# Kernel tuning notes

Hardware: AMD Instinct MI355X
Metric: run time of the kernel (lower is better)

## Reference

```python
import jax, jax.numpy as jnp
import numpy as np

N, C_IN, T, V = 16, 64, 512, 22
C_OUT = 256
INTER = C_OUT // 4  # coff_embedding = 4


def setup_inputs() -> dict:
    key = jax.random.key(0)
    ks = jax.random.split(key, 8)
    x = jax.random.normal(ks[0], (N, C_IN, T, V), dtype=jnp.float32)
    A = jax.random.uniform(ks[1], (N, T, V, V), dtype=jnp.float32)
    # 1x1 conv weights (only subset 0 is used in forward)
    Wa = jax.random.normal(ks[2], (INTER, C_IN), dtype=jnp.float32) * (2.0 / C_IN) ** 0.5
    ba = jnp.zeros((INTER,), dtype=jnp.float32)
    Wb = jax.random.normal(ks[3], (INTER, C_IN), dtype=jnp.float32) * (2.0 / C_IN) ** 0.5
    bb = jnp.zeros((INTER,), dtype=jnp.float32)
    Wd = jax.random.normal(ks[4], (C_OUT, C_IN), dtype=jnp.float32) * (2.0 / (C_OUT * 3)) ** 0.5
    bd = jnp.zeros((C_OUT,), dtype=jnp.float32)
    return {"x": x, "A": A, "Wa": Wa, "ba": ba, "Wb": Wb, "bb": bb, "Wd": Wd, "bd": bd}


def reference(x, A, Wa, ba, Wb, bb, Wd, bd):
    # x: (N,C,T,V); A: (N,T,V,V). All T frames batched (original loops over t).
    inter = Wa.shape[0]
    # 1x1 convs over channel dim
    A1 = jnp.einsum('ic,nctv->nitv', Wa, x) + ba[None, :, None, None]  # (N,inter,T,V)
    A2 = jnp.einsum('ic,nctv->nitv', Wb, x) + bb[None, :, None, None]
    # scores[n,t,u,v] = sum_i A1[n,i,t,u] * A2[n,i,t,v], scaled by inter channels
    scores = jnp.einsum('nitu,nitv->ntuv', A1, A2) / inter
    # torch Softmax(dim=-2): over rows (u axis)
    A_dyn = jax.nn.softmax(scores, axis=-2)
    # forward-created PA is constant 1e-6 added to A
    A_comb = A + 1e-6 + A_dyn  # (N,T,V,V)
    # graph aggregation: z[n,c,t,u] = sum_w A_comb[n,t,u,w] * x[n,c,t,w]
    z = jnp.einsum('ntuw,nctw->nctu', A_comb, x)
    out = jnp.einsum('oc,nctv->notv', Wd, z) + bd[None, :, None, None]  # (N,C_out,T,V)
    return jax.nn.relu(out)
```

## Files before the change

kernel.cpp:

```cpp
#include <hip/hip_runtime.h>

#define NB    16
#define CIN   64
#define TT    512
#define VV    22
#define COUT  256
#define TBK   4
#define NTB   (TT / TBK)
#define ZROW  (TBK * VV)
#define PAD   24
#define OPAD  23

typedef __attribute__((ext_vector_type(8))) short bf16x8;
typedef __attribute__((ext_vector_type(4))) float f32x4;

__device__ __forceinline__ ushort f2bf(float f) {
    unsigned u = __float_as_uint(f);
    return (ushort)((u + 0x7FFFu + ((u >> 16) & 1u)) >> 16);
}
__device__ __forceinline__ uint pk2(float a, float b) {
    return (uint)f2bf(a) | ((uint)f2bf(b) << 16);
}

__global__ void w_to_bf16(const float* __restrict__ Wa, const float* __restrict__ Wb,
                          const float* __restrict__ Wd,
                          ushort* __restrict__ WaB, ushort* __restrict__ WbB,
                          ushort* __restrict__ WdB)
{
    int i = blockIdx.x * 256 + threadIdx.x;
    if (i < CIN * CIN)                 WaB[i] = f2bf(Wa[i]);
    else if (i < 2 * CIN * CIN)        WbB[i - CIN * CIN] = f2bf(Wb[i - CIN * CIN]);
    else if (i < 2 * CIN * CIN + COUT * CIN)
                                       WdB[i - 2 * CIN * CIN] = f2bf(Wd[i - 2 * CIN * CIN]);
}

__global__ __launch_bounds__(256, 3) void agcn_fused_mfma(
    const float* __restrict__ x, const float* __restrict__ A,
    const ushort* __restrict__ WaB, const float* __restrict__ ba,
    const ushort* __restrict__ WbB, const float* __restrict__ bb,
    const ushort* __restrict__ WdB, const float* __restrict__ bd,
    float* __restrict__ out)
{
    const int bx = blockIdx.x;
    const int tq = (bx & 7) * 16 + (bx >> 3);
    const int n  = blockIdx.y;
    const int tid = threadIdx.x;
    const int lane = tid & 63, wave = tid >> 6;
    const int hi = lane >> 4, lo = lane & 15;
    const int t0 = tq * TBK;

    __shared__ __align__(16) ushort xsb[TBK * 64 * 32];
    __shared__ __align__(16) ushort frag[11264];
    ushort* xbf   = frag;
    ushort* A1bf  = frag;
    ushort* A2bf  = frag + 5632;
    ushort* z_lds = frag;
    ushort* psb   = frag + 6144;
    ushort* zbf   = xsb;

    for (int i = tid; i < TBK * 64 * 5; i += 256) {
        int row = i / 5, q = i - row * 5;
        reinterpret_cast<uint*>(&xsb[row * 32 + 22])[q] = 0u;
    }

    {
        const float* xsrc = x + ((size_t)n * CIN * TT + t0) * VV;
        for (int i4 = tid; i4 < CIN * 22; i4 += 256) {
            int c = i4 / 22, q = i4 - c * 22;
            float4 v4 = *reinterpret_cast<const float4*>(xsrc + (size_t)c * (TT * VV) + q * 4);
            #pragma unroll
            for (int j = 0; j < 4; ++j) {
                int e  = q * 4 + j;
                int tt = e / 22, v = e - tt * 22;
                float val = (j == 0) ? v4.x : (j == 1) ? v4.y : (j == 2) ? v4.z : v4.w;
                xsb[(tt * 64 + c) * 32 + v] = f2bf(val);
            }
        }
    }
    __syncthreads();

    for (int it = tid; it < 1024; it += 256) {
        int kb = it >> 9;
        int t  = (it >> 7) & 3;
        int nt = (it >> 6) & 1;
        int ln = it & 63;
        int v  = nt * 16 + (ln & 15);
        int c0 = kb * 32 + (ln >> 4) * 8;
        ushort tmp[8];
        #pragma unroll
        for (int j = 0; j < 8; ++j) tmp[j] = xsb[(t * 64 + c0 + j) * 32 + v];
        *reinterpret_cast<uint4*>(&xbf[(size_t)it * 8]) = *reinterpret_cast<const uint4*>(tmp);
    }
    __syncthreads();

    f32x4 acc_a[TBK][2], acc_b[TBK][2];
    {
        const int m0 = wave * 16;
        float bav[4], bbv[4];
        #pragma unroll
        for (int r = 0; r < 4; ++r) { bav[r] = ba[m0 + hi * 4 + r]; bbv[r] = bb[m0 + hi * 4 + r]; }
        #pragma unroll
        for (int t = 0; t < TBK; ++t)
            #pragma unroll
            for (int nt = 0; nt < 2; ++nt)
                #pragma unroll
                for (int r = 0; r < 4; ++r) { acc_a[t][nt][r] = bav[r]; acc_b[t][nt][r] = bbv[r]; }
        #pragma unroll
        for (int kb = 0; kb < 2; ++kb) {
            bf16x8 awa = *reinterpret_cast<const bf16x8*>(&WaB[(size_t)(m0 + lo) * CIN + kb * 32 + hi * 8]);
            bf16x8 awb = *reinterpret_cast<const bf16x8*>(&WbB[(size_t)(m0 + lo) * CIN + kb * 32 + hi * 8]);
            #pragma unroll
            for (int t = 0; t < TBK; ++t) {
                #pragma unroll
                for (int nt = 0; nt < 2; ++nt) {
                    bf16x8 bf = *reinterpret_cast<const bf16x8*>(
                        &xbf[(((size_t)(kb * 4 + t) * 2 + nt) * 64 + lane) * 8]);
                    acc_a[t][nt] = __builtin_amdgcn_mfma_f32_16x16x32_bf16(awa, bf, acc_a[t][nt], 0, 0, 0);
                    acc_b[t][nt] = __builtin_amdgcn_mfma_f32_16x16x32_bf16(awb, bf, acc_b[t][nt], 0, 0, 0);
                }
            }
        }
    }
    __syncthreads();

    {
        const int m0 = wave * 16;
        #pragma unroll
        for (int t = 0; t < TBK; ++t) {
            #pragma unroll
            for (int nt = 0; nt < 2; ++nt) {
                const int u = nt * 16 + lo;
                if (u < VV) {
                    uint2 va = {pk2(acc_a[t][nt][0], acc_a[t][nt][1]),
                                pk2(acc_a[t][nt][2], acc_a[t][nt][3])};
                    uint2 vb = {pk2(acc_b[t][nt][0], acc_b[t][nt][1]),
                                pk2(acc_b[t][nt][2], acc_b[t][nt][3])};
                    *reinterpret_cast<uint2*>(&A1bf[((size_t)t * VV + u) * 64 + m0 + hi * 4]) = va;
                    *reinterpret_cast<uint2*>(&A2bf[((size_t)t * VV + u) * 64 + m0 + hi * 4]) = vb;
                }
            }
        }
    }
    __syncthreads();

    f32x4 s[2][2];
    {
        const int t = wave;
        bf16x8 zfrag;
        #pragma unroll
        for (int j = 0; j < 8; ++j) zfrag[j] = 0;
        #pragma unroll
        for (int mt = 0; mt < 2; ++mt)
            #pragma unroll
            for (int nt = 0; nt < 2; ++nt)
                #pragma unroll
                for (int r = 0; r < 4; ++r) s[mt][nt][r] = 0.f;
        #pragma unroll
        for (int kb = 0; kb < 2; ++kb) {
            bf16x8 a[2], b2[2];
            #pragma unroll
            for (int mt = 0; mt < 2; ++mt) {
                const int row = mt * 16 + lo;
                a[mt] = (row < VV) ? *reinterpret_cast<const bf16x8*>(
                            &A1bf[((size_t)t * VV + row) * 64 + kb * 32 + hi * 8]) : zfrag;
            }
            #pragma unroll
            for (int nt = 0; nt < 2; ++nt) {
                const int row = nt * 16 + lo;
                b2[nt] = (row < VV) ? *reinterpret_cast<const bf16x8*>(
                            &A2bf[((size_t)t * VV + row) * 64 + kb * 32 + hi * 8]) : zfrag;
            }
            #pragma unroll
            for (int mt = 0; mt < 2; ++mt)
                #pragma unroll
                for (int nt = 0; nt < 2; ++nt)
                    s[mt][nt] = __builtin_amdgcn_mfma_f32_16x16x32_bf16(a[mt], b2[nt], s[mt][nt], 0, 0, 0);
        }
    }
    __syncthreads();

    {
        const int t = wave;
        bf16x8 zfrag;
        #pragma unroll
        for (int j = 0; j < 8; ++j) zfrag[j] = 0;

        {
            uint* pz = reinterpret_cast<uint*>(psb + (size_t)t * VV * 32);
            #pragma unroll
            for (int i = 0; i < 6; ++i) {
                int idx = i * 64 + lane;
                if (idx < (VV * 32) / 2) pz[idx] = 0u;
            }
        }

        float m[2] = {-1e30f, -1e30f};
        #pragma unroll
        for (int mt = 0; mt < 2; ++mt)
            #pragma unroll
            for (int nt = 0; nt < 2; ++nt)
                #pragma unroll
                for (int r = 0; r < 4; ++r) {
                    s[mt][nt][r] *= (1.0f / 64.0f);
                    const int u = mt * 16 + hi * 4 + r;
                    if (u < VV) m[nt] = fmaxf(m[nt], s[mt][nt][r]);
                }
        #pragma unroll
        for (int nt = 0; nt < 2; ++nt) {
            m[nt] = fmaxf(m[nt], __shfl_xor(m[nt], 16));
            m[nt] = fmaxf(m[nt], __shfl_xor(m[nt], 32));
        }
        float e[2][2][4];
        float sum[2] = {0.f, 0.f};
        #pragma unroll
        for (int mt = 0; mt < 2; ++mt)
            #pragma unroll
            for (int nt = 0; nt < 2; ++nt)
                #pragma unroll
                for (int r = 0; r < 4; ++r) {
                    const int u = mt * 16 + hi * 4 + r;
                    float ev = (u < VV) ? __expf(s[mt][nt][r] - m[nt]) : 0.f;
                    e[mt][nt][r] = ev;
                    sum[nt] += ev;
                }
        #pragma unroll
        for (int nt = 0; nt < 2; ++nt) {
            sum[nt] += __shfl_xor(sum[nt], 16);
            sum[nt] += __shfl_xor(sum[nt], 32);
        }

        {
            const float* Ag = A + ((size_t)(n * TT + t0 + t) * VV) * VV;
            #pragma unroll
            for (int nt = 0; nt < 2; ++nt) {
                const int v = nt * 16 + lo;
                if (v < VV) {
                    const float inv = 1.0f / sum[nt];
                    #pragma unroll
                    for (int mt = 0; mt < 2; ++mt)
                        #pragma unroll
                        for (int r = 0; r < 4; ++r) {
                            const int u = mt * 16 + hi * 4 + r;
                            if (u < VV)
                                psb[((size_t)t * VV + u) * 32 + v] =
                                    f2bf(Ag[u * VV + v] + 1e-6f + e[mt][nt][r] * inv);
                        }
                }
            }
        }
        {
            bf16x8 bfr[2];
            #pragma unroll
            for (int nt = 0; nt < 2; ++nt) {
                const int u = nt * 16 + lo;
                bfr[nt] = (u < VV) ? *reinterpret_cast<const bf16x8*>(
                              &psb[((size_t)t * VV + u) * 32 + hi * 8]) : zfrag;
            }
            #pragma unroll
            for (int mt = 0; mt < 4; ++mt) {
                bf16x8 a = *reinterpret_cast<const bf16x8*>(
                    &xsb[((size_t)(t * 64 + mt * 16 + lo)) * 32 + hi * 8]);
                #pragma unroll
                for (int nt = 0; nt < 2; ++nt) {
                    f32x4 acc = {0.f, 0.f, 0.f, 0.f};
                    acc = __builtin_amdgcn_mfma_f32_16x16x32_bf16(a, bfr[nt], acc, 0, 0, 0);
                    const int u = nt * 16 + lo;
                    if (u < VV) {
                        #pragma unroll
                        for (int r = 0; r < 4; ++r) {
                            const int c = mt * 16 + hi * 4 + r;
                            z_lds[(size_t)c * 96 + t * VV + u] = f2bf(acc[r]);
                        }
                    }
                }
            }
        }
    }
    __syncthreads();

    for (int it = tid; it < 768; it += 256) {
        const int kb  = it / 384;
        const int rem = it - kb * 384;
        const int nt  = rem >> 6;
        const int ln  = rem & 63;
        const int tv  = nt * 16 + (ln & 15);
        const int c0  = kb * 32 + (ln >> 4) * 8;
        ushort tmp[8];
        if (tv < ZROW) {
            #pragma unroll
            for (int j = 0; j < 8; ++j) tmp[j] = z_lds[(size_t)(c0 + j) * 96 + tv];
        } else {
            #pragma unroll
            for (int j = 0; j < 8; ++j) tmp[j] = 0;
        }
        *reinterpret_cast<uint4*>(&zbf[(size_t)it * 8]) = *reinterpret_cast<const uint4*>(tmp);
    }
    __syncthreads();

    {
        const int o0 = wave * 64;
        f32x4 acc[4][6];
        #pragma unroll
        for (int mt = 0; mt < 4; ++mt) {
            #pragma unroll
            for (int r = 0; r < 4; ++r) {
                const float b = bd[o0 + mt * 16 + hi * 4 + r];
                #pragma unroll
                for (int nt = 0; nt < 6; ++nt) acc[mt][nt][r] = b;
            }
        }
        #pragma unroll
        for (int kb = 0; kb < 2; ++kb) {
            bf16x8 bfr[6];
            #pragma unroll
            for (int nt = 0; nt < 6; ++nt)
                bfr[nt] = *reinterpret_cast<const bf16x8*>(&zbf[((kb * 6 + nt) * 64 + lane) * 8]);
            #pragma unroll
            for (int mt = 0; mt < 4; ++mt) {
                bf16x8 aw = *reinterpret_cast<const bf16x8*>(
                    &WdB[(size_t)(o0 + mt * 16 + lo) * CIN + kb * 32 + hi * 8]);
                #pragma unroll
                for (int nt = 0; nt < 6; ++nt)
                    acc[mt][nt] = __builtin_amdgcn_mfma_f32_16x16x32_bf16(aw, bfr[nt], acc[mt][nt], 0, 0, 0);
            }
        }
        #pragma unroll
        for (int mt = 0; mt < 4; ++mt) {
            #pragma unroll
            for (int nt = 0; nt < 6; ++nt) {
                const int col = nt * 16 + lo;
                if (col < ZROW) {
                    #pragma unroll
                    for (int r = 0; r < 4; ++r) {
                        const int o = o0 + mt * 16 + hi * 4 + r;
                        out[((size_t)(n * COUT + o)) * (TT * VV) + (size_t)tq * ZROW + col]
                            = fmaxf(acc[mt][nt][r], 0.f);
                    }
                }
            }
        }
    }
}

__global__ __launch_bounds__(256, 4) void agcn_fused(
    const float* __restrict__ x, const float* __restrict__ A,
    const float* __restrict__ Wa, const float* __restrict__ ba,
    const float* __restrict__ Wb, const float* __restrict__ bb,
    const float* __restrict__ Wd, const float* __restrict__ bd,
    float* __restrict__ out)
{
    const int t   = blockIdx.x;
    const int n   = blockIdx.y;
    const int tid = threadIdx.x;
    __shared__ float smem[7424];
    float* xs   = smem;
    float* A1s  = smem + 1536;
    float* A2s  = smem + 3072;
    float* Ssf  = smem + 4608;
    float* Psf  = smem + 5136;
    float* outs = smem;
    float* zs   = smem + 5888;

    for (int f = tid; f < CIN * VV; f += 256) {
        int c = f / VV, v = f - c * VV;
        xs[c * PAD + v] = x[(((size_t)n * CIN + c) * TT + t) * VV + v];
    }
    {
        const float* Ag = A + (((size_t)n * TT + t) * VV) * VV;
        for (int f = tid; f < VV * VV; f += 256) {
            int u = f / VV, v = f - u * VV;
            Psf[u * PAD + v] = Ag[f] + 1e-6f;
        }
    }
    __syncthreads();
    {
        const int r  = tid & 63;
        const int q  = tid >> 6;
        const int us = (q * VV) >> 2;
        const int ue = ((q + 1) * VV) >> 2;
        const float* War = Wa + r * CIN;
        const float* Wbr = Wb + r * CIN;
        float acc1[6], acc2[6];
        const float b1 = ba[r], b2 = bb[r];
        #pragma unroll
        for (int u = 0; u < 6; ++u) { acc1[u] = b1; acc2[u] = b2; }
        for (int c = 0; c < CIN; c += 4) {
            float4 wa4 = *reinterpret_cast<const float4*>(War + c);
            float4 wb4 = *reinterpret_cast<const float4*>(Wbr + c);
            #pragma unroll
            for (int u = 0; u < 6; ++u) {
                float x0 = xs[(c + 0) * PAD + us + u];
                float x1 = xs[(c + 1) * PAD + us + u];
                float x2 = xs[(c + 2) * PAD + us + u];
                float x3 = xs[(c + 3) * PAD + us + u];
                acc1[u] += wa4.x * x0 + wa4.y * x1 + wa4.z * x2 + wa4.w * x3;
                acc2[u] += wb4.x * x0 + wb4.y * x1 + wb4.z * x2 + wb4.w * x3;
            }
        }
        #pragma unroll
        for (int u = 0; u < 6; ++u) {
            if (us + u < ue) {
                A1s[r * PAD + us + u] = acc1[u];
                A2s[r * PAD + us + u] = acc2[u];
            }
        }
    }
    __syncthreads();
    for (int f = tid; f < VV * VV; f += 256) {
        int u = f / VV, v = f - u * VV;
        float s = 0.f;
        for (int i = 0; i < CIN; ++i)
            s += A1s[i * PAD + u] * A2s[i * PAD + v];
        Ssf[u * PAD + v] = s * (1.0f / 64.0f);
    }
    __syncthreads();
    if (tid < VV) {
        const int v = tid;
        float m = -1e30f;
        #pragma unroll
        for (int u = 0; u < VV; ++u) m = fmaxf(m, Ssf[u * PAD + v]);
        float sum = 0.f;
        #pragma unroll
        for (int u = 0; u < VV; ++u) sum += __expf(Ssf[u * PAD + v] - m);
        const float inv = 1.0f / sum;
        #pragma unroll
        for (int u = 0; u < VV; ++u)
            Psf[u * PAD + v] += __expf(Ssf[u * PAD + v] - m) * inv;
    }
    __syncthreads();
    for (int f = tid; f < CIN * VV; f += 256) {
        int c = f / VV, u = f - c * VV;
        float s = 0.f;
        #pragma unroll
        for (int w = 0; w < VV; ++w)
            s += Psf[u * PAD + w] * xs[c * PAD + w];
        zs[c * PAD + u] = s;
    }
    __syncthreads();
    {
        const int o = tid;
        const float* Wr = Wd + o * CIN;
        float acc[VV];
        const float b = bd[o];
        #pragma unroll
        for (int u = 0; u < VV; ++u) acc[u] = b;
        for (int c = 0; c < CIN; c += 4) {
            float4 w4 = *reinterpret_cast<const float4*>(Wr + c);
            #pragma unroll
            for (int cc = 0; cc < 4; ++cc) {
                const float w = (cc == 0) ? w4.x : (cc == 1) ? w4.y : (cc == 2) ? w4.z : w4.w;
                const float* zr = zs + (c + cc) * PAD;
                #pragma unroll
                for (int uq = 0; uq < 5; ++uq) {
                    float4 zq = *reinterpret_cast<const float4*>(zr + uq * 4);
                    acc[uq * 4 + 0] += w * zq.x;
                    acc[uq * 4 + 1] += w * zq.y;
                    acc[uq * 4 + 2] += w * zq.z;
                    acc[uq * 4 + 3] += w * zq.w;
                }
                float2 zt = *reinterpret_cast<const float2*>(zr + 20);
                acc[20] += w * zt.x;
                acc[21] += w * zt.y;
            }
        }
        #pragma unroll
        for (int u = 0; u < VV; ++u)
            outs[o * OPAD + u] = fmaxf(acc[u], 0.f);
    }
    __syncthreads();
    {
        const size_t obase = (size_t)n * COUT * TT * VV + (size_t)t * VV;
        for (int f = tid; f < COUT * VV; f += 256) {
            int o = f / VV, u = f - o * VV;
            out[obase + (size_t)o * (TT * VV) + u] = outs[o * OPAD + u];
        }
    }
}

extern "C" void kernel_launch(void* const* d_in, const int* in_sizes, int n_in,
                              void* d_out, int out_size, void* d_ws, size_t ws_size,
                              hipStream_t stream) {
    const float* x  = (const float*)d_in[0];
    const float* A  = (const float*)d_in[1];
    const float* Wa = (const float*)d_in[2];
    const float* ba = (const float*)d_in[3];
    const float* Wb = (const float*)d_in[4];
    const float* bb = (const float*)d_in[5];
    const float* Wd = (const float*)d_in[6];
    const float* bd = (const float*)d_in[7];
    float* outp     = (float*)d_out;

    const size_t wab_bytes = (size_t)CIN * CIN * sizeof(ushort);
    const size_t wdb_bytes = (size_t)COUT * CIN * sizeof(ushort);

    if (ws_size >= 2 * wab_bytes + wdb_bytes) {
        ushort* wab = (ushort*)d_ws;
        ushort* wbb = (ushort*)((char*)d_ws + wab_bytes);
        ushort* wdb = (ushort*)((char*)d_ws + 2 * wab_bytes);
        const int prep_items = 2 * CIN * CIN + COUT * CIN;
        w_to_bf16<<<(prep_items + 255) / 256, 256, 0, stream>>>(Wa, Wb, Wd, wab, wbb, wdb);
        dim3 g(NTB, NB);
        agcn_fused_mfma<<<g, 256, 0, stream>>>(x, A, wab, ba, wbb, bb, wdb, bd, outp);
    } else {
        dim3 grid(TT, NB);
        agcn_fused<<<grid, 256, 0, stream>>>(x, A, Wa, ba, Wb, bb, Wd, bd, outp);
    }
}
```

Before: 75.03 us.

## Process eight frames per block with 512 threads and split A1/A2 projections across waves

Doubles the temporal tile from 4 to 8 frames per block and doubles the block to 512 threads (8 waves). Half the waves compute the Wa projection and half the Wb projection instead of each wave computing both. With 176 columns fitting exactly into 11 MFMA tiles, the final Wd GEMM drops its padded columns and loops over column tiles, which reduces register pressure and makes output rows longer and contiguous. The cost is twice the LDS per block and fewer blocks (1024), which may lower occupancy and latency hiding.

```diff
diff --git a/kernel.cpp b/kernel.cpp
--- a/kernel.cpp
+++ b/kernel.cpp
@@ -5,7 +5,7 @@
 #define TT    512
 #define VV    22
 #define COUT  256
-#define TBK   4
+#define TBK   8
 #define NTB   (TT / TBK)
 #define ZROW  (TBK * VV)
 #define PAD   24
@@ -34,7 +34,7 @@
                                        WdB[i - 2 * CIN * CIN] = f2bf(Wd[i - 2 * CIN * CIN]);
 }
 
-__global__ __launch_bounds__(256, 3) void agcn_fused_mfma(
+__global__ __launch_bounds__(512, 2) void agcn_fused_mfma(
     const float* __restrict__ x, const float* __restrict__ A,
     const ushort* __restrict__ WaB, const float* __restrict__ ba,
     const ushort* __restrict__ WbB, const float* __restrict__ bb,
@@ -42,7 +42,7 @@
     float* __restrict__ out)
 {
     const int bx = blockIdx.x;
-    const int tq = (bx & 7) * 16 + (bx >> 3);
+    const int tq = (bx & 7) * 8 + (bx >> 3);
     const int n  = blockIdx.y;
     const int tid = threadIdx.x;
     const int lane = tid & 63, wave = tid >> 6;
@@ -50,23 +50,23 @@
     const int t0 = tq * TBK;
 
     __shared__ __align__(16) ushort xsb[TBK * 64 * 32];
-    __shared__ __align__(16) ushort frag[11264];
+    __shared__ __align__(16) ushort frag[22528];
     ushort* xbf   = frag;
     ushort* A1bf  = frag;
-    ushort* A2bf  = frag + 5632;
+    ushort* A2bf  = frag + 11264;
     ushort* z_lds = frag;
-    ushort* psb   = frag + 6144;
+    ushort* psb   = frag + 11264;
     ushort* zbf   = xsb;
 
-    for (int i = tid; i < TBK * 64 * 5; i += 256) {
+    for (int i = tid; i < TBK * 64 * 5; i += 512) {
         int row = i / 5, q = i - row * 5;
         reinterpret_cast<uint*>(&xsb[row * 32 + 22])[q] = 0u;
     }
 
     {
         const float* xsrc = x + ((size_t)n * CIN * TT + t0) * VV;
-        for (int i4 = tid; i4 < CIN * 22; i4 += 256) {
-            int c = i4 / 22, q = i4 - c * 22;
+        for (int i4 = tid; i4 < CIN * 44; i4 += 512) {
+            int c = i4 / 44, q = i4 - c * 44;
             float4 v4 = *reinterpret_cast<const float4*>(xsrc + (size_t)c * (TT * VV) + q * 4);
             #pragma unroll
             for (int j = 0; j < 4; ++j) {
@@ -79,9 +79,9 @@
     }
     __syncthreads();
 
-    for (int it = tid; it < 1024; it += 256) {
-        int kb = it >> 9;
-        int t  = (it >> 7) & 3;
+    for (int it = tid; it < 2048; it += 512) {
+        int kb = it >> 10;
+        int t  = (it >> 7) & 7;
         int nt = (it >> 6) & 1;
         int ln = it & 63;
         int v  = nt * 16 + (ln & 15);
@@ -93,50 +93,50 @@
     }
     __syncthreads();
 
-    f32x4 acc_a[TBK][2], acc_b[TBK][2];
-    {
-        const int m0 = wave * 16;
-        float bav[4], bbv[4];
-        #pragma unroll
-        for (int r = 0; r < 4; ++r) { bav[r] = ba[m0 + hi * 4 + r]; bbv[r] = bb[m0 + hi * 4 + r]; }
+    f32x4 acc[TBK][2];
+    {
+        const int isB = wave >> 2;
+        const int m0  = (wave & 3) * 16;
+        const ushort* W  = isB ? WbB : WaB;
+        const float*  bv = isB ? bb  : ba;
+        float bias[4];
+        #pragma unroll
+        for (int r = 0; r < 4; ++r) bias[r] = bv[m0 + hi * 4 + r];
         #pragma unroll
         for (int t = 0; t < TBK; ++t)
             #pragma unroll
             for (int nt = 0; nt < 2; ++nt)
                 #pragma unroll
-                for (int r = 0; r < 4; ++r) { acc_a[t][nt][r] = bav[r]; acc_b[t][nt][r] = bbv[r]; }
+                for (int r = 0; r < 4; ++r) acc[t][nt][r] = bias[r];
         #pragma unroll
         for (int kb = 0; kb < 2; ++kb) {
-            bf16x8 awa = *reinterpret_cast<const bf16x8*>(&WaB[(size_t)(m0 + lo) * CIN + kb * 32 + hi * 8]);
-            bf16x8 awb = *reinterpret_cast<const bf16x8*>(&WbB[(size_t)(m0 + lo) * CIN + kb * 32 + hi * 8]);
+            bf16x8 aw = *reinterpret_cast<const bf16x8*>(&W[(size_t)(m0 + lo) * CIN + kb * 32 + hi * 8]);
             #pragma unroll
             for (int t = 0; t < TBK; ++t) {
                 #pragma unroll
                 for (int nt = 0; nt < 2; ++nt) {
                     bf16x8 bf = *reinterpret_cast<const bf16x8*>(
-                        &xbf[(((size_t)(kb * 4 + t) * 2 + nt) * 64 + lane) * 8]);
-                    acc_a[t][nt] = __builtin_amdgcn_mfma_f32_16x16x32_bf16(awa, bf, acc_a[t][nt], 0, 0, 0);
-                    acc_b[t][nt] = __builtin_amdgcn_mfma_f32_16x16x32_bf16(awb, bf, acc_b[t][nt], 0, 0, 0);
-                }
-            }
-        }
-    }
-    __syncthreads();
-
-    {
-        const int m0 = wave * 16;
+                        &xbf[(((size_t)(kb * 8 + t) * 2 + nt) * 64 + lane) * 8]);
+                    acc[t][nt] = __builtin_amdgcn_mfma_f32_16x16x32_bf16(aw, bf, acc[t][nt], 0, 0, 0);
+                }
+            }
+        }
+    }
+    __syncthreads();
+
+    {
+        const int isB = wave >> 2;
+        const int m0  = (wave & 3) * 16;
+        ushort* dst = isB ? A2bf : A1bf;
         #pragma unroll
         for (int t = 0; t < TBK; ++t) {
             #pragma unroll
             for (int nt = 0; nt < 2; ++nt) {
                 const int u = nt * 16 + lo;
                 if (u < VV) {
-                    uint2 va = {pk2(acc_a[t][nt][0], acc_a[t][nt][1]),
-                                pk2(acc_a[t][nt][2], acc_a[t][nt][3])};
-                    uint2 vb = {pk2(acc_b[t][nt][0], acc_b[t][nt][1]),
-                                pk2(acc_b[t][nt][2], acc_b[t][nt][3])};
-                    *reinterpret_cast<uint2*>(&A1bf[((size_t)t * VV + u) * 64 + m0 + hi * 4]) = va;
-                    *reinterpret_cast<uint2*>(&A2bf[((size_t)t * VV + u) * 64 + m0 + hi * 4]) = vb;
+                    uint2 va = {pk2(acc[t][nt][0], acc[t][nt][1]),
+                                pk2(acc[t][nt][2], acc[t][nt][3])};
+                    *reinterpret_cast<uint2*>(&dst[((size_t)t * VV + u) * 64 + m0 + hi * 4]) = va;
                 }
             }
         }
@@ -262,14 +262,14 @@
                     &xsb[((size_t)(t * 64 + mt * 16 + lo)) * 32 + hi * 8]);
                 #pragma unroll
                 for (int nt = 0; nt < 2; ++nt) {
-                    f32x4 acc = {0.f, 0.f, 0.f, 0.f};
-                    acc = __builtin_amdgcn_mfma_f32_16x16x32_bf16(a, bfr[nt], acc, 0, 0, 0);
+                    f32x4 acc4 = {0.f, 0.f, 0.f, 0.f};
+                    acc4 = __builtin_amdgcn_mfma_f32_16x16x32_bf16(a, bfr[nt], acc4, 0, 0, 0);
                     const int u = nt * 16 + lo;
                     if (u < VV) {
                         #pragma unroll
                         for (int r = 0; r < 4; ++r) {
                             const int c = mt * 16 + hi * 4 + r;
-                            z_lds[(size_t)c * 96 + t * VV + u] = f2bf(acc[r]);
+                            z_lds[(size_t)c * ZROW + t * VV + u] = f2bf(acc4[r]);
                         }
                     }
                 }
@@ -278,64 +278,57 @@
     }
     __syncthreads();
 
-    for (int it = tid; it < 768; it += 256) {
-        const int kb  = it / 384;
-        const int rem = it - kb * 384;
+    for (int it = tid; it < 1408; it += 512) {
+        const int kb  = it / 704;
+        const int rem = it - kb * 704;
         const int nt  = rem >> 6;
         const int ln  = rem & 63;
         const int tv  = nt * 16 + (ln & 15);
         const int c0  = kb * 32 + (ln >> 4) * 8;
         ushort tmp[8];
-        if (tv < ZROW) {
-            #pragma unroll
-            for (int j = 0; j < 8; ++j) tmp[j] = z_lds[(size_t)(c0 + j) * 96 + tv];
-        } else {
-            #pragma unroll
-            for (int j = 0; j < 8; ++j) tmp[j] = 0;
-        }
+        #pragma unroll
+        for (int j = 0; j < 8; ++j) tmp[j] = z_lds[(size_t)(c0 + j) * ZROW + tv];
         *reinterpret_cast<uint4*>(&zbf[(size_t)it * 8]) = *reinterpret_cast<const uint4*>(tmp);
     }
     __syncthreads();
 
     {
-        const int o0 = wave * 64;
-        f32x4 acc[4][6];
-        #pragma unroll
-        for (int mt = 0; mt < 4; ++mt) {
-            #pragma unroll
-            for (int r = 0; r < 4; ++r) {
-                const float b = bd[o0 + mt * 16 + hi * 4 + r];
-                #pragma unroll
-                for (int nt = 0; nt < 6; ++nt) acc[mt][nt][r] = b;
-            }
-        }
-        #pragma unroll
-        for (int kb = 0; kb < 2; ++kb) {
-            bf16x8 bfr[6];
-            #pragma unroll
-            for (int nt = 0; nt < 6; ++nt)
-                bfr[nt] = *reinterpret_cast<const bf16x8*>(&zbf[((kb * 6 + nt) * 64 + lane) * 8]);
-            #pragma unroll
-            for (int mt = 0; mt < 4; ++mt) {
-                bf16x8 aw = *reinterpret_cast<const bf16x8*>(
+        const int o0 = wave * 32;
+        float bdv[2][4];
+        #pragma unroll
+        for (int mt = 0; mt < 2; ++mt)
+            #pragma unroll
+            for (int r = 0; r < 4; ++r)
+                bdv[mt][r] = bd[o0 + mt * 16 + hi * 4 + r];
+        bf16x8 aw[2][2];
+        #pragma unroll
+        for (int kb = 0; kb < 2; ++kb)
+            #pragma unroll
+            for (int mt = 0; mt < 2; ++mt)
+                aw[kb][mt] = *reinterpret_cast<const bf16x8*>(
                     &WdB[(size_t)(o0 + mt * 16 + lo) * CIN + kb * 32 + hi * 8]);
-                #pragma unroll
-                for (int nt = 0; nt < 6; ++nt)
-                    acc[mt][nt] = __builtin_amdgcn_mfma_f32_16x16x32_bf16(aw, bfr[nt], acc[mt][nt], 0, 0, 0);
-            }
-        }
-        #pragma unroll
-        for (int mt = 0; mt < 4; ++mt) {
-            #pragma unroll
-            for (int nt = 0; nt < 6; ++nt) {
-                const int col = nt * 16 + lo;
-                if (col < ZROW) {
-                    #pragma unroll
-                    for (int r = 0; r < 4; ++r) {
-                        const int o = o0 + mt * 16 + hi * 4 + r;
-                        out[((size_t)(n * COUT + o)) * (TT * VV) + (size_t)tq * ZROW + col]
-                            = fmaxf(acc[mt][nt][r], 0.f);
-                    }
+
+        for (int nt = 0; nt < 11; ++nt) {
+            f32x4 acc2[2];
+            #pragma unroll
+            for (int mt = 0; mt < 2; ++mt)
+                #pragma unroll
+                for (int r = 0; r < 4; ++r) acc2[mt][r] = bdv[mt][r];
+            #pragma unroll
+            for (int kb = 0; kb < 2; ++kb) {
+                bf16x8 bfr = *reinterpret_cast<const bf16x8*>(&zbf[((kb * 11 + nt) * 64 + lane) * 8]);
+                #pragma unroll
+                for (int mt = 0; mt < 2; ++mt)
+                    acc2[mt] = __builtin_amdgcn_mfma_f32_16x16x32_bf16(aw[kb][mt], bfr, acc2[mt], 0, 0, 0);
+            }
+            const int col = nt * 16 + lo;
+            #pragma unroll
+            for (int mt = 0; mt < 2; ++mt) {
+                #pragma unroll
+                for (int r = 0; r < 4; ++r) {
+                    const int o = o0 + mt * 16 + hi * 4 + r;
+                    out[((size_t)(n * COUT + o)) * (TT * VV) + (size_t)tq * ZROW + col]
+                        = fmaxf(acc2[mt][r], 0.f);
                 }
             }
         }
@@ -500,7 +493,7 @@
         const int prep_items = 2 * CIN * CIN + COUT * CIN;
         w_to_bf16<<<(prep_items + 255) / 256, 256, 0, stream>>>(Wa, Wb, Wd, wab, wbb, wdb);
         dim3 g(NTB, NB);
-        agcn_fused_mfma<<<g, 256, 0, stream>>>(x, A, wab, ba, wbb, bb, wdb, bd, outp);
+        agcn_fused_mfma<<<g, 512, 0, stream>>>(x, A, wab, ba, wbb, bb, wdb, bd, outp);
     } else {
         dim3 grid(TT, NB);
         agcn_fused<<<grid, 256, 0, stream>>>(x, A, Wa, ba, Wb, bb, Wd, bd, outp);
```

New measurement: 62.84 us. -16.3%, faster.
